# Kernel optimization log

Hardware: AMD Instinct MI355X
Metric: run time of the kernel (lower is better)

The kernel has to match this reference:

```python
import jax, jax.numpy as jnp
import numpy as np

B, T, C = 2, 4096, 1024
NH, HS, BD, DELTA = 16, 64, 16, 32  # n_head, head_size, bond_dim, horizon window


def setup_inputs() -> dict:
    key = jax.random.key(0)
    ks = jax.random.split(key, 10)
    s = lambda k, shape: jax.random.normal(k, shape, jnp.float32) * 0.02
    return {
        "x": jax.random.normal(ks[0], (B, T, C), jnp.float32),
        "W_disp": s(ks[1], (C, NH * BD)),          # W_disp (no bias)
        "W_val": s(ks[2], (C, C)),                  # W_val (no bias)
        "rel_pos_emb": s(ks[3], (DELTA, BD)),       # rel pos embedding table
        "W_pos": s(ks[4], (BD, BD)),                # pos_proj (no bias)
        "W_sf": s(ks[5], (BD, 2 * BD)),             # strain_fused weight
        "b_sf": jnp.zeros((2 * BD,), jnp.float32),  # strain_fused bias
        "w_bond": s(ks[6], (BD,)),                  # bond_out (no bias)
        "w_dmg": s(ks[7], (BD,)),                   # damage_out weight
        "b_dmg": jnp.full((), -3.0, jnp.float32),   # damage_out bias init -3.0
        "W_cproj": s(ks[8], (C, C)),                # c_proj (no bias)
    }


def reference(x, W_disp, W_val, rel_pos_emb, W_pos, W_sf, b_sf, w_bond, w_dmg, b_dmg, W_cproj):
    Bb, Tt, Cc = x.shape
    delta = DELTA
    gelu = lambda v: jax.nn.gelu(v, approximate=False)

    # projections -> (B, nh, T, *)
    disp = (x @ W_disp).reshape(Bb, Tt, NH, BD).transpose(0, 2, 1, 3)
    val = (x @ W_val).reshape(Bb, Tt, NH, HS).transpose(0, 2, 1, 3)

    idx = jnp.arange(Tt)[:, None] + jnp.arange(delta)[None, :]  # (T, delta) into padded axis
    dpad = jnp.pad(disp, ((0, 0), (0, 0), (delta - 1, 0), (0, 0)))
    win = dpad[:, :, idx, :]                      # (B, nh, T, delta, bd)
    strain = win - disp[:, :, :, None, :]

    pos_feat = rel_pos_emb @ W_pos                # (delta, bd)
    fused = strain @ W_sf + b_sf                  # (B, nh, T, delta, 2bd)
    bf, df = fused[..., :BD], fused[..., BD:]
    bond_logits = gelu(bf + pos_feat) @ w_bond    # (B, nh, T, delta)
    damage = jax.nn.sigmoid(gelu(df) @ w_dmg + b_dmg)
    scores = bond_logits - damage * 10.0

    # causal/left-edge mask: kv_pos = t - delta + 1 + j >= 0
    cmask = (jnp.arange(Tt)[:, None] - delta + 1 + jnp.arange(delta)[None, :]) >= 0
    scores = jnp.where(cmask, scores, -jnp.inf)
    weights = jax.nn.softmax(scores, axis=-1)     # (B, nh, T, delta)

    vpad = jnp.pad(val, ((0, 0), (0, 0), (delta - 1, 0), (0, 0)))
    vw = vpad[:, :, idx, :]                       # (B, nh, T, delta, hs)
    out = jnp.einsum('bntj,bntjh->bnth', weights, vw)
    out = out.transpose(0, 2, 1, 3).reshape(Bb, Tt, Cc)
    return out @ W_cproj                          # resid dropout is eval no-op
```

## Files before the change

kernel.cpp:

```cpp
#include <hip/hip_runtime.h>
#include <hip/hip_bf16.h>

#define BB 2
#define TT 4096
#define CC 1024
#define NH 16
#define HS 64
#define BD 16
#define DELTA 32

typedef unsigned short u16;
typedef unsigned int u32;
typedef __bf16 bf16x8 __attribute__((ext_vector_type(8)));
typedef float floatx4 __attribute__((ext_vector_type(4)));

__device__ __forceinline__ float bf2f(u16 u) {
    unsigned v = ((unsigned)u) << 16;
    return __builtin_bit_cast(float, v);
}
__device__ __forceinline__ u16 f2bf(float x) {
    unsigned u = __builtin_bit_cast(unsigned, x);
    unsigned r = u + 0x7fffu + ((u >> 16) & 1u);
    return (u16)(r >> 16);
}
__device__ __forceinline__ float rcpf(float x) {
    float r;
    asm("v_rcp_f32 %0, %1" : "=v"(r) : "v"(x));
    return r;
}

__device__ __forceinline__ void storeC(float* p, float v) { *p = v; }
__device__ __forceinline__ void storeC(u16* p, float v) { *p = f2bf(v); }

#define GC0 0.3989422804014327f
#define GC1 (-0.06649038006690546f)
#define GC2 0.009973557010035818f
__device__ __forceinline__ float gelup(float x) {
    float u = x * x;
    float p = fmaf(u, fmaf(u, GC2, GC1), GC0);
    return x * fmaf(x, p, 0.5f);
}

__device__ __forceinline__ void load16_lds(const u16* g, u16* l) {
    __builtin_amdgcn_global_load_lds(
        (const __attribute__((address_space(1))) void*)g,
        (__attribute__((address_space(3))) void*)l, 16, 0, 0);
}

__global__ __launch_bounds__(256) void convert_x(
    const float* __restrict__ in, u16* __restrict__ out, long n4)
{
    long i = (long)blockIdx.x * 256 + threadIdx.x;
    if (i >= n4) return;
    float4 v = ((const float4*)in)[i];
    ushort4 o;
    o.x = f2bf(v.x); o.y = f2bf(v.y); o.z = f2bf(v.z); o.w = f2bf(v.w);
    ((ushort4*)out)[i] = o;
}

__global__ __launch_bounds__(256) void prep_kernel(
    const float* __restrict__ Wdisp, const float* __restrict__ Wsf,
    const float* __restrict__ rel,   const float* __restrict__ Wpos,
    u16* __restrict__ WcatT, float* __restrict__ posf)
{
    int bi = blockIdx.x;
    if (bi < 512) {
        int n = bi >> 5, o = bi & 31;
        float wcol[16];
        #pragma unroll
        for (int d = 0; d < 16; ++d) wcol[d] = Wsf[d * 32 + o];
        for (int c = threadIdx.x; c < CC; c += 256) {
            float acc = 0.f;
            #pragma unroll
            for (int d = 0; d < 16; ++d)
                acc += Wdisp[c * (NH * BD) + n * 16 + d] * wcol[d];
            WcatT[(long)bi * CC + c] = f2bf(acc);
        }
    } else {
        for (int e = threadIdx.x; e < DELTA * BD; e += 256) {
            int j = e >> 4, o2 = e & 15;
            float acc = 0.f;
            #pragma unroll
            for (int d = 0; d < 16; ++d)
                acc += rel[j * 16 + d] * Wpos[d * 16 + o2];
            posf[e] = acc;
        }
    }
}

__global__ __launch_bounds__(256) void transpose_cvt(
    const float* __restrict__ in, u16* __restrict__ out, int dim)
{
    __shared__ u16 tile[32][33];
    int tx = threadIdx.x, ty = threadIdx.y;
    int x = blockIdx.x * 32 + tx;
    #pragma unroll
    for (int i = 0; i < 4; ++i) {
        int y = blockIdx.y * 32 + ty + i * 8;
        tile[ty + i * 8][tx] = f2bf(in[(long)y * dim + x]);
    }
    __syncthreads();
    int x2 = blockIdx.y * 32 + tx;
    #pragma unroll
    for (int i = 0; i < 4; ++i) {
        int y2 = blockIdx.x * 32 + ty + i * 8;
        out[(long)y2 * dim + x2] = tile[tx][ty + i * 8];
    }
}

template <typename OUT_T>
__global__ __launch_bounds__(256) void gemm_bt(
    const u16* __restrict__ A, const u16* __restrict__ Bt,
    OUT_T* __restrict__ C, int M, int N, int K)
{
    __shared__ __align__(16) u16 sA[128 * 64];
    __shared__ __align__(16) u16 sB[128 * 64];

    const int tid  = threadIdx.x;
    const int lane = tid & 63;
    const int wave = tid >> 6;
    const int wr = wave >> 1, wc = wave & 1;

    const u32 lin   = blockIdx.y * gridDim.x + blockIdx.x;
    const u32 total = gridDim.x * gridDim.y;
    const u32 qch   = total >> 3;
    const u32 nl    = (lin & 7) * qch + (lin >> 3);
    const int bx    = nl % gridDim.x;
    const int by    = nl / gridDim.x;
    const int m0 = by * 128;
    const int n0 = bx * 128;

    const int sg = tid & 7;
    const int sr = tid >> 3;

    floatx4 acc[4][4] = {};

    for (int k0 = 0; k0 < K; k0 += 64) {
        __syncthreads();
        #pragma unroll
        for (int rnd = 0; rnd < 4; ++rnd) {
            const int r = sr + rnd * 32;
            const int gsw = sg ^ (r & 7);
            load16_lds(A  + (long)(m0 + r) * K + k0 + gsw * 8,
                       &sA[rnd * 2048 + wave * 512]);
            load16_lds(Bt + (long)(n0 + r) * K + k0 + gsw * 8,
                       &sB[rnd * 2048 + wave * 512]);
        }
        __syncthreads();

        #pragma unroll
        for (int kh = 0; kh < 2; ++kh) {
            bf16x8 aF[4], bF[4];
            #pragma unroll
            for (int mt = 0; mt < 4; ++mt) {
                const int rr = wr * 64 + mt * 16 + (lane & 15);
                const int g = (kh * 4 + (lane >> 4)) ^ (rr & 7);
                aF[mt] = *(const bf16x8*)&sA[rr * 64 + g * 8];
            }
            #pragma unroll
            for (int nt = 0; nt < 4; ++nt) {
                const int rr = wc * 64 + nt * 16 + (lane & 15);
                const int g = (kh * 4 + (lane >> 4)) ^ (rr & 7);
                bF[nt] = *(const bf16x8*)&sB[rr * 64 + g * 8];
            }
            #pragma unroll
            for (int mt = 0; mt < 4; ++mt)
                #pragma unroll
                for (int nt = 0; nt < 4; ++nt)
                    acc[mt][nt] = __builtin_amdgcn_mfma_f32_16x16x32_bf16(
                        aF[mt], bF[nt], acc[mt][nt], 0, 0, 0);
        }
    }

    const int rbase = (lane >> 4) << 2;
    const int ccol  = lane & 15;
    #pragma unroll
    for (int mt = 0; mt < 4; ++mt)
        #pragma unroll
        for (int nt = 0; nt < 4; ++nt)
            #pragma unroll
            for (int r = 0; r < 4; ++r) {
                int m  = m0 + wr * 64 + mt * 16 + rbase + r;
                int nn = n0 + wc * 64 + nt * 16 + ccol;
                storeC(C + (long)m * N + nn, acc[mt][nt][r]);
            }
}

__global__ __launch_bounds__(512) void attn_kernel(
    const u16* __restrict__ xcat,
    const float* __restrict__ posf,
    const float* __restrict__ b_sf, const float* __restrict__ w_bond,
    const float* __restrict__ w_dmg, const float* __restrict__ b_dmg,
    u16* __restrict__ att)
{
    __shared__ __align__(16) float sGs[63][36];
    __shared__ __align__(16) float sBias[32][36];
    __shared__ __align__(16) u16 sVT[64 * 64];
    __shared__ __align__(16) u16 sWb[32 * 64];
    __shared__ __align__(16) float sWBv[16], sWDv[16];

    const int tid = threadIdx.x;
    const int t_local = tid >> 5;
    const int j = tid & 31;
    const int t0 = blockIdx.x * 32;
    const int n = blockIdx.y;
    const int b = blockIdx.z;
    const long bT = (long)b * TT;

    const u32* xc = (const u32*)xcat;

    for (int e = tid; e < 63 * 16; e += 512) {
        int r = e >> 4, c = e & 15;
        int tok = t0 - 31 + r;
        u32 w = (tok >= 0) ? xc[(bT + tok) * 768 + n * 16 + c] : 0u;
        float2 f2 = make_float2(bf2f((u16)(w & 0xffffu)), bf2f((u16)(w >> 16)));
        *(float2*)&sGs[r][2 * c] = f2;
    }
    u32* sVT32 = (u32*)sVT;
    for (int e = tid; e < 32 * 32; e += 512) {
        int c = e & 31, rp = e >> 5;
        int tok0 = t0 - 31 + 2 * rp, tok1 = tok0 + 1;
        u32 a  = (tok0 >= 0 && tok0 < TT) ? xc[(bT + tok0) * 768 + 256 + n * 32 + c] : 0u;
        u32 bb = (tok1 >= 0 && tok1 < TT) ? xc[(bT + tok1) * 768 + 256 + n * 32 + c] : 0u;
        u32 lo = (a & 0xffffu) | (bb << 16);
        u32 hi = (a >> 16) | (bb & 0xffff0000u);
        int h0 = 2 * c, h1 = 2 * c + 1;
        int wd0 = (rp & 3) | ((((rp >> 2) ^ h0) & 7) << 2);
        int wd1 = (rp & 3) | ((((rp >> 2) ^ h1) & 7) << 2);
        sVT32[h0 * 32 + wd0] = lo;
        sVT32[h1 * 32 + wd1] = hi;
    }
    u32* sWb32 = (u32*)sWb;
    for (int e = tid; e < 32 * 32; e += 512) sWb32[e] = 0u;
    for (int e = tid; e < 1024; e += 512) {
        int jj = e >> 5, o = e & 31;
        sBias[jj][o] = b_sf[o] + ((o < 16) ? posf[jj * 16 + o] : 0.f);
    }
    if (tid < 16)      sWBv[tid]      = w_bond[tid];
    else if (tid < 32) sWDv[tid - 16] = w_dmg[tid - 16];
    __syncthreads();

    const float bdmg = b_dmg[0];
    float4 bb4[8];
    #pragma unroll
    for (int q = 0; q < 8; ++q) bb4[q] = *(const float4*)&sBias[j][4 * q];

    #pragma unroll
    for (int th = 0; th < 2; ++th) {
        const int tl = t_local + 16 * th;
        const float* Sp = sGs[tl + j];
        const float* Tp = sGs[tl + 31];
        const bool valid = (t0 + tl + j) >= 31;

        float bond = 0.f, dmg = 0.f;
        #pragma unroll
        for (int q = 0; q < 4; ++q) {
            float4 s = *(const float4*)&Sp[4 * q];
            float4 t = *(const float4*)&Tp[4 * q];
            float4 w = *(const float4*)&sWBv[4 * q];
            float4 bbv = bb4[q];
            bond += gelup(s.x - t.x + bbv.x) * w.x;
            bond += gelup(s.y - t.y + bbv.y) * w.y;
            bond += gelup(s.z - t.z + bbv.z) * w.z;
            bond += gelup(s.w - t.w + bbv.w) * w.w;
        }
        #pragma unroll
        for (int q = 0; q < 4; ++q) {
            float4 s = *(const float4*)&Sp[16 + 4 * q];
            float4 t = *(const float4*)&Tp[16 + 4 * q];
            float4 w = *(const float4*)&sWDv[4 * q];
            float4 bbv = bb4[4 + q];
            dmg += gelup(s.x - t.x + bbv.x) * w.x;
            dmg += gelup(s.y - t.y + bbv.y) * w.y;
            dmg += gelup(s.z - t.z + bbv.z) * w.z;
            dmg += gelup(s.w - t.w + bbv.w) * w.w;
        }
        float damage = rcpf(1.f + __expf(-(dmg + bdmg)));
        float score = bond - 10.f * damage;
        float p = valid ? __expf(score) : 0.f;
        float sum = p;
        #pragma unroll
        for (int off = 16; off; off >>= 1) sum += __shfl_xor(sum, off, 32);
        const int k = tl + j;
        const int kk = ((((k >> 3) ^ tl) & 7) << 3) | (k & 7);
        sWb[tl * 64 + kk] = f2bf(p * rcpf(sum));
    }
    __syncthreads();

    const int wave = tid >> 6;
    const int lane = tid & 63;
    const int ttile = wave & 1;
    const int htile = wave >> 1;
    const int fr = lane & 15;
    const int q4 = lane >> 4;
    const int h = htile * 16 + fr;
    const int r = ttile * 16 + fr;

    floatx4 o4 = {0.f, 0.f, 0.f, 0.f};
    #pragma unroll
    for (int ks = 0; ks < 2; ++ks) {
        const int ga = (ks * 4 + q4) ^ (r & 7);
        bf16x8 aF = *(const bf16x8*)&sWb[r * 64 + ga * 8];
        const int gb = (ks * 4 + q4) ^ (h & 7);
        bf16x8 bF = *(const bf16x8*)&sVT[h * 64 + gb * 8];
        o4 = __builtin_amdgcn_mfma_f32_16x16x32_bf16(aF, bF, o4, 0, 0, 0);
    }
    const int trow = ttile * 16 + (q4 << 2);
    const int col = n * 64 + htile * 16 + fr;
    #pragma unroll
    for (int rr = 0; rr < 4; ++rr)
        att[(bT + t0 + trow + rr) * 1024 + col] = f2bf(o4[rr]);
}

extern "C" void kernel_launch(void* const* d_in, const int* in_sizes, int n_in,
                              void* d_out, int out_size, void* d_ws, size_t ws_size,
                              hipStream_t stream)
{
    const float* x      = (const float*)d_in[0];
    const float* Wdisp  = (const float*)d_in[1];
    const float* Wval   = (const float*)d_in[2];
    const float* rel    = (const float*)d_in[3];
    const float* Wpos   = (const float*)d_in[4];
    const float* Wsf    = (const float*)d_in[5];
    const float* bsf    = (const float*)d_in[6];
    const float* wbond  = (const float*)d_in[7];
    const float* wdmg   = (const float*)d_in[8];
    const float* bdmg   = (const float*)d_in[9];
    const float* Wcproj = (const float*)d_in[10];

    char* ws = (char*)d_ws;
    const size_t O_WCAT = 0;
    const size_t O_WCPT = (size_t)4 << 20;
    const size_t O_POSF = (size_t)6 << 20;
    const size_t O_XBF  = (size_t)8 << 20;
    const size_t O_XCAT = (size_t)24 << 20;
    const size_t O_ATT  = (size_t)48 << 20;

    u16*   WcatT = (u16*)(ws + O_WCAT);
    u16*   WcpT  = (u16*)(ws + O_WCPT);
    float* posf  = (float*)(ws + O_POSF);
    u16*   xbf   = (u16*)(ws + O_XBF);
    u16*   xcat  = (u16*)(ws + O_XCAT);
    u16*   att   = (u16*)(ws + O_ATT);

    const int M = BB * TT;
    const long n4 = (long)M * CC / 4;

    convert_x<<<(int)((n4 + 255) / 256), 256, 0, stream>>>(x, xbf, n4);
    prep_kernel<<<513, 256, 0, stream>>>(Wdisp, Wsf, rel, Wpos, WcatT, posf);
    transpose_cvt<<<dim3(32, 32), dim3(32, 8), 0, stream>>>(Wval, WcatT + (size_t)512 * 1024, 1024);
    transpose_cvt<<<dim3(32, 32), dim3(32, 8), 0, stream>>>(Wcproj, WcpT, 1024);

    gemm_bt<u16><<<dim3(1536 / 128, M / 128), 256, 0, stream>>>(xbf, WcatT, xcat, M, 1536, CC);
    attn_kernel<<<dim3(TT / 32, NH, BB), 512, 0, stream>>>(xcat, posf, bsf, wbond, wdmg, bdmg, att);
    gemm_bt<float><<<dim3(1024 / 128, M / 128), 256, 0, stream>>>(att, WcpT, (float*)d_out, M, 1024, CC);
}
```

Baseline: 212.6 us.

## Rewrite GEMM as 128x256 tile with double-buffered LDS ping-pong pipeline

Rewrites the bf16 GEMM used for both projections. Each block is now 512 threads computing a 128x256 output tile instead of 256 threads on 128x128. Global-to-LDS loads go into two buffers so the next K slice is fetched while MFMAs run on the current one, with explicit vmcnt/lgkmcnt waits, barriers and s_setprio around the MFMA bursts. The larger tile halves the number of blocks (384 and 256), which may leave some of the 256 CUs idle. The hand-written wait counts also make correctness depend on exact load ordering.

```diff
diff --git a/kernel.cpp b/kernel.cpp
--- a/kernel.cpp
+++ b/kernel.cpp
@@ -108,18 +108,68 @@
     }
 }
 
+#define STAGE_A_(P, T, H) do { \
+    const int r_ = tid >> 3; \
+    load16_lds(A + (long)(m0 + (H)*64 + r_) * K + (T)*64 + (((tid & 7) ^ (r_ & 7)) << 3), \
+               &sA[P][(H)*4096 + wave*512]); } while (0)
+
+#define STAGE_B_(P, T, H) do { \
+    _Pragma("unroll") \
+    for (int i_ = 0; i_ < 2; ++i_) { \
+        const int r_ = i_*64 + (tid >> 3); \
+        load16_lds(Bt + (long)(n0 + (H)*128 + r_) * K + (T)*64 + (((tid & 7) ^ (r_ & 7)) << 3), \
+                   &sB[P][(H)*8192 + i_*4096 + wave*512]); } } while (0)
+
+#define LDB_(P) do { \
+    _Pragma("unroll") \
+    for (int n_ = 0; n_ < 4; ++n_) { \
+        const int rr_ = wc*64 + n_*16 + fr; \
+        _Pragma("unroll") \
+        for (int kk_ = 0; kk_ < 2; ++kk_) { \
+            const int pg_ = ((kk_ << 2) | q4) ^ (rr_ & 7); \
+            bF[n_][kk_] = *(const bf16x8*)&sB[P][rr_*64 + pg_*8]; } } } while (0)
+
+#define LDA2_(P, QA, QB) do { \
+    _Pragma("unroll") \
+    for (int kk_ = 0; kk_ < 2; ++kk_) { \
+        int rr_ = wr*64 + (QA)*16 + fr; \
+        int pg_ = ((kk_ << 2) | q4) ^ (rr_ & 7); \
+        aF[0][kk_] = *(const bf16x8*)&sA[P][rr_*64 + pg_*8]; \
+        rr_ = wr*64 + (QB)*16 + fr; \
+        pg_ = ((kk_ << 2) | q4) ^ (rr_ & 7); \
+        aF[1][kk_] = *(const bf16x8*)&sA[P][rr_*64 + pg_*8]; } } while (0)
+
+#define MFMA16_(QA, QB) do { \
+    _Pragma("unroll") \
+    for (int n_ = 0; n_ < 4; ++n_) { \
+        _Pragma("unroll") \
+        for (int kk_ = 0; kk_ < 2; ++kk_) { \
+            acc[QA][n_] = __builtin_amdgcn_mfma_f32_16x16x32_bf16( \
+                aF[0][kk_], bF[n_][kk_], acc[QA][n_], 0, 0, 0); \
+            acc[QB][n_] = __builtin_amdgcn_mfma_f32_16x16x32_bf16( \
+                aF[1][kk_], bF[n_][kk_], acc[QB][n_], 0, 0, 0); } } } while (0)
+
+#define BAR_    __builtin_amdgcn_s_barrier()
+#define LGKM0_  do { asm volatile("s_waitcnt lgkmcnt(0)" ::: "memory"); \
+                     __builtin_amdgcn_sched_barrier(0); } while (0)
+#define VMC4_   asm volatile("s_waitcnt vmcnt(4)" ::: "memory")
+#define VMC0_   asm volatile("s_waitcnt vmcnt(0)" ::: "memory")
+
 template <typename OUT_T>
-__global__ __launch_bounds__(256) void gemm_bt(
+__global__ __launch_bounds__(512, 2) void gemm_bt(
     const u16* __restrict__ A, const u16* __restrict__ Bt,
     OUT_T* __restrict__ C, int M, int N, int K)
 {
-    __shared__ __align__(16) u16 sA[128 * 64];
-    __shared__ __align__(16) u16 sB[128 * 64];
+    __shared__ __align__(16) u16 sA[2][128 * 64];
+    __shared__ __align__(16) u16 sB[2][256 * 64];
 
     const int tid  = threadIdx.x;
     const int lane = tid & 63;
     const int wave = tid >> 6;
-    const int wr = wave >> 1, wc = wave & 1;
+    const int wr = wave >> 2;
+    const int wc = wave & 3;
+    const int fr = lane & 15;
+    const int q4 = lane >> 4;
 
     const u32 lin   = blockIdx.y * gridDim.x + blockIdx.x;
     const u32 total = gridDim.x * gridDim.y;
@@ -128,63 +178,74 @@
     const int bx    = nl % gridDim.x;
     const int by    = nl / gridDim.x;
     const int m0 = by * 128;
-    const int n0 = bx * 128;
-
-    const int sg = tid & 7;
-    const int sr = tid >> 3;
+    const int n0 = bx * 256;
 
     floatx4 acc[4][4] = {};
-
-    for (int k0 = 0; k0 < K; k0 += 64) {
-        __syncthreads();
+    bf16x8 bF[4][2];
+    bf16x8 aF[2][2];
+
+    STAGE_B_(0, 0, 0); STAGE_B_(0, 0, 1);
+    STAGE_A_(0, 0, 0); STAGE_A_(0, 0, 1);
+    STAGE_B_(1, 1, 0); STAGE_B_(1, 1, 1);
+    VMC4_;
+    BAR_;
+
+    const int nIter = K >> 7;
+    for (int it = 0, t = 0; it < nIter; ++it, t += 2) {
+        const bool full = (it < nIter - 1);
+
+        LDB_(0);
+        LDA2_(0, 0, 1);
+        STAGE_A_(1, t + 1, 0);
+        STAGE_A_(1, t + 1, 1);
+        BAR_; LGKM0_;
+        __builtin_amdgcn_s_setprio(1); MFMA16_(0, 1); __builtin_amdgcn_s_setprio(0);
+        BAR_;
+
+        LDA2_(0, 2, 3);
+        if (full) { STAGE_B_(0, t + 2, 0); STAGE_B_(0, t + 2, 1); }
+        BAR_; LGKM0_;
+        __builtin_amdgcn_s_setprio(1); MFMA16_(2, 3); __builtin_amdgcn_s_setprio(0);
+        if (full) { VMC4_; } else { VMC0_; }
+        BAR_;
+
+        LDB_(1);
+        LDA2_(1, 0, 1);
+        if (full) { STAGE_A_(0, t + 2, 0); STAGE_A_(0, t + 2, 1); }
+        BAR_; LGKM0_;
+        __builtin_amdgcn_s_setprio(1); MFMA16_(0, 1); __builtin_amdgcn_s_setprio(0);
+        BAR_;
+
+        LDA2_(1, 2, 3);
+        if (full) { STAGE_B_(1, t + 3, 0); STAGE_B_(1, t + 3, 1); }
+        BAR_; LGKM0_;
+        __builtin_amdgcn_s_setprio(1); MFMA16_(2, 3); __builtin_amdgcn_s_setprio(0);
+        if (full) { VMC4_; }
+        BAR_;
+    }
+
+    const int rbase = q4 << 2;
+    #pragma unroll
+    for (int q = 0; q < 4; ++q)
         #pragma unroll
-        for (int rnd = 0; rnd < 4; ++rnd) {
-            const int r = sr + rnd * 32;
-            const int gsw = sg ^ (r & 7);
-            load16_lds(A  + (long)(m0 + r) * K + k0 + gsw * 8,
-                       &sA[rnd * 2048 + wave * 512]);
-            load16_lds(Bt + (long)(n0 + r) * K + k0 + gsw * 8,
-                       &sB[rnd * 2048 + wave * 512]);
-        }
-        __syncthreads();
-
-        #pragma unroll
-        for (int kh = 0; kh < 2; ++kh) {
-            bf16x8 aF[4], bF[4];
-            #pragma unroll
-            for (int mt = 0; mt < 4; ++mt) {
-                const int rr = wr * 64 + mt * 16 + (lane & 15);
-                const int g = (kh * 4 + (lane >> 4)) ^ (rr & 7);
-                aF[mt] = *(const bf16x8*)&sA[rr * 64 + g * 8];
-            }
-            #pragma unroll
-            for (int nt = 0; nt < 4; ++nt) {
-                const int rr = wc * 64 + nt * 16 + (lane & 15);
-                const int g = (kh * 4 + (lane >> 4)) ^ (rr & 7);
-                bF[nt] = *(const bf16x8*)&sB[rr * 64 + g * 8];
-            }
-            #pragma unroll
-            for (int mt = 0; mt < 4; ++mt)
-                #pragma unroll
-                for (int nt = 0; nt < 4; ++nt)
-                    acc[mt][nt] = __builtin_amdgcn_mfma_f32_16x16x32_bf16(
-                        aF[mt], bF[nt], acc[mt][nt], 0, 0, 0);
-        }
-    }
-
-    const int rbase = (lane >> 4) << 2;
-    const int ccol  = lane & 15;
-    #pragma unroll
-    for (int mt = 0; mt < 4; ++mt)
-        #pragma unroll
-        for (int nt = 0; nt < 4; ++nt)
+        for (int n = 0; n < 4; ++n)
             #pragma unroll
             for (int r = 0; r < 4; ++r) {
-                int m  = m0 + wr * 64 + mt * 16 + rbase + r;
-                int nn = n0 + wc * 64 + nt * 16 + ccol;
-                storeC(C + (long)m * N + nn, acc[mt][nt][r]);
+                int m  = m0 + wr * 64 + q * 16 + rbase + r;
+                int nn = n0 + wc * 64 + n * 16 + fr;
+                storeC(C + (long)m * N + nn, acc[q][n][r]);
             }
 }
+
+#undef STAGE_A_
+#undef STAGE_B_
+#undef LDB_
+#undef LDA2_
+#undef MFMA16_
+#undef BAR_
+#undef LGKM0_
+#undef VMC4_
+#undef VMC0_
 
 __global__ __launch_bounds__(512) void attn_kernel(
     const u16* __restrict__ xcat,
@@ -351,7 +412,7 @@
     transpose_cvt<<<dim3(32, 32), dim3(32, 8), 0, stream>>>(Wval, WcatT + (size_t)512 * 1024, 1024);
     transpose_cvt<<<dim3(32, 32), dim3(32, 8), 0, stream>>>(Wcproj, WcpT, 1024);
 
-    gemm_bt<u16><<<dim3(1536 / 128, M / 128), 256, 0, stream>>>(xbf, WcatT, xcat, M, 1536, CC);
+    gemm_bt<u16><<<dim3(1536 / 256, M / 128), 512, 0, stream>>>(xbf, WcatT, xcat, M, 1536, CC);
     attn_kernel<<<dim3(TT / 32, NH, BB), 512, 0, stream>>>(xcat, posf, bsf, wbond, wdmg, bdmg, att);
-    gemm_bt<float><<<dim3(1024 / 128, M / 128), 256, 0, stream>>>(att, WcpT, (float*)d_out, M, 1024, CC);
-}
+    gemm_bt<float><<<dim3(1024 / 256, M / 128), 512, 0, stream>>>(att, WcpT, (float*)d_out, M, 1024, CC);
+}
```

Measured after the change: 228.4 us. 7.4% more time.
